# Kernel tuning notes

Hardware: AMD Instinct MI355X
Metric: run time of the kernel (lower is better)

## Reference

```python
import jax, jax.numpy as jnp
import numpy as np

G, N = 1024, 40            # graphs, nodes per graph (complete graphs)
SLOPE = 0.1                # leaky relu negative slope
SMAT_IDX = jnp.array([0, 1, 2, 3, 1, 4, 5, 6, 2, 5, 7, 8, 3, 6, 8, 9])


def setup_inputs() -> dict:
    key = jax.random.key(0)
    ks = jax.random.split(key, 24)

    # --- graph structure: G identical complete graphs of N nodes ---
    ii, jj = np.meshgrid(np.arange(N), np.arange(N), indexing="ij")
    mask = ii != jj
    src_l, dst_l = ii[mask], jj[mask]              # directed edges per graph
    offs = (np.arange(G) * N)[:, None]
    edge_index = np.stack([(src_l[None] + offs).ravel(),
                           (dst_l[None] + offs).ravel()]).astype(np.int64)
    iu, ju = np.triu_indices(N, 1)
    M = iu.shape[0]                                 # 780 undirected edges
    ud_edges = np.stack([iu, ju], 1).astype(np.int64)
    edge_map = np.zeros((N, N), np.int64)
    edge_map[iu, ju] = np.arange(M)
    edge_map[ju, iu] = np.arange(M)

    def w(k, shape, fan_in):
        return jax.random.normal(k, shape, jnp.float32) / np.sqrt(fan_in)

    inp = {
        "x": jax.random.normal(ks[0], (G * N, 16), jnp.float32),
        "edge_index": jnp.asarray(edge_index),
        "ud_edges": jnp.asarray(ud_edges),
        "edge_map": jnp.asarray(edge_map),
        # GCN stack 6->32->32->64
        "Wg0": w(ks[1], (6, 32), 6),   "bg0": jnp.zeros((32,), jnp.float32),
        "Wg1": w(ks[2], (32, 32), 32), "bg1": jnp.zeros((32,), jnp.float32),
        "Wg2": w(ks[3], (32, 64), 32), "bg2": jnp.zeros((64,), jnp.float32),
        # node MLP 64->64->64->10
        "Wn0": w(ks[4], (64, 64), 64), "bn0": jnp.zeros((64,), jnp.float32),
        "Wn1": w(ks[5], (64, 64), 64), "bn1": jnp.zeros((64,), jnp.float32),
        "Wn2": w(ks[6], (64, 10), 64), "bn2": jnp.zeros((10,), jnp.float32),
        # edge MLP 64->64->64->10
        "We0": w(ks[7], (64, 64), 64), "be0": jnp.zeros((64,), jnp.float32),
        "We1": w(ks[8], (64, 64), 64), "be1": jnp.zeros((64,), jnp.float32),
        "We2": w(ks[9], (64, 10), 64), "be2": jnp.zeros((10,), jnp.float32),
    }
    return inp


def _forward(x, edge_index, ud_edges, edge_map,
             Wg0, bg0, Wg1, bg1, Wg2, bg2,
             Wn0, bn0, Wn1, bn1, Wn2, bn2,
             We0, be0, We1, be1, We2, be2):
    num_nodes = x.shape[0]
    h = x[:, :6]                                   # node_feature_mode == 1
    src, dst = edge_index[0], edge_index[1]

    # GCN normalization (add_self_loops=False, edge_weight=1)
    deg = jax.ops.segment_sum(jnp.ones(src.shape[0], x.dtype), dst,
                              num_segments=num_nodes)
    dis = jnp.where(deg > 0, jax.lax.rsqrt(jnp.maximum(deg, 1e-12)), 0.0)
    norm = dis[src] * dis[dst]                     # [E]

    def gcn(h, W, b):
        m = (h @ W)[src] * norm[:, None]
        return jax.ops.segment_sum(m, dst, num_segments=num_nodes) + b

    # eval mode: dropout is identity
    h = jax.nn.leaky_relu(gcn(h, Wg0, bg0), SLOPE)
    h = jax.nn.leaky_relu(gcn(h, Wg1, bg1), SLOPE)
    h = gcn(h, Wg2, bg2)                           # [G*N, 64]

    hg = h.reshape(G, N, -1)                       # [G, N, 64]

    def mlp(z, Ws, bs):
        for W, b in zip(Ws[:-1], bs[:-1]):
            z = jax.nn.leaky_relu(z @ W + b, SLOPE)
        return z @ Ws[-1] + bs[-1]

    vp = mlp(hg, [Wn0, Wn1, Wn2], [bn0, bn1, bn2])            # [G, N, 10]
    e = hg[:, ud_edges[:, 0], :] + hg[:, ud_edges[:, 1], :]   # [G, M, 64]
    ep = mlp(e, [We0, We1, We2], [be0, be1, be2])             # [G, M, 10]

    # recover_X: diag blocks smat(vp[i]), off-diag smat(ep[edge_map[i,j]])
    epm = ep[:, edge_map, :]                                  # [G, N, N, 10]
    eye = jnp.eye(N, dtype=bool)[None, :, :, None]
    vecs = jnp.where(eye, vp[:, :, None, :], epm)             # [G, N, N, 10]
    blocks = vecs[..., SMAT_IDX].reshape(G, N, N, 4, 4)
    X = blocks.transpose(0, 1, 3, 2, 4).reshape(G, 4 * N, 4 * N)
    return h, X


def reference(x, edge_index, ud_edges, edge_map,
              Wg0, bg0, Wg1, bg1, Wg2, bg2,
              Wn0, bn0, Wn1, bn1, Wn2, bn2,
              We0, be0, We1, be1, We2, be2):
    return _forward(x, edge_index, ud_edges, edge_map,
                    Wg0, bg0, Wg1, bg1, Wg2, bg2,
                    Wn0, bn0, Wn1, bn1, Wn2, bn2,
                    We0, be0, We1, be1, We2, be2)
```

## Files before the change

kernel.cpp:

```cpp
#include <hip/hip_runtime.h>

#define G_GRAPHS 1024
#define N_NODES  40
#define M_EDGES  780
#define NUM_NODES (G_GRAPHS * N_NODES)
#define H_ELEMS  (NUM_NODES * 64)
#define X_STRIDE 160
#define X_PER_G  25600
#define SLOPE 0.1f

#define PACK_PER_MLP 9216

typedef __bf16 bf16x8 __attribute__((ext_vector_type(8)));
typedef unsigned short us8 __attribute__((ext_vector_type(8)));
typedef float f32x4 __attribute__((ext_vector_type(4)));

__device__ __forceinline__ float lrelu(float v) { return fmaxf(v, SLOPE * v); }
__device__ __forceinline__ unsigned short f2bf(float x) {
    __bf16 b = (__bf16)x;
    return __builtin_bit_cast(unsigned short, b);
}
__device__ __forceinline__ unsigned int pk2bf(float a, float b) {
    return (unsigned int)f2bf(a) | ((unsigned int)f2bf(b) << 16);
}

__global__ __launch_bounds__(256) void k_prep(const float* __restrict__ We0,
                                              const float* __restrict__ We1,
                                              const float* __restrict__ We2,
                                              const float* __restrict__ Wn0,
                                              const float* __restrict__ Wn1,
                                              const float* __restrict__ Wn2,
                                              unsigned short* __restrict__ wp) {
    int t = blockIdx.x * 256 + threadIdx.x;
    int mlp = t / PACK_PER_MLP;
    int o = t - mlp * PACK_PER_MLP;
    const float* W0 = mlp ? Wn0 : We0;
    const float* W1 = mlp ? Wn1 : We1;
    const float* W2 = mlp ? Wn2 : We2;
    float val;
    if (o < 8192) {
        const float* W = (o < 4096) ? W0 : W1;
        int idx = o & 4095;
        int j = idx & 7, l = (idx >> 3) & 63, tt = idx >> 9;
        int kt = tt & 1, mt = tt >> 1;
        int k = kt * 32 + ((l >> 4) & 3) * 8 + j;
        int m = mt * 16 + (l & 15);
        val = W[k * 64 + m];
    } else {
        int idx = o - 8192;
        int j = idx & 7, l = (idx >> 3) & 63, kt = idx >> 9;
        int k = kt * 32 + ((l >> 4) & 3) * 8 + j;
        int m = l & 15;
        val = (m < 10) ? W2[k * 10 + m] : 0.f;
    }
    wp[mlp * PACK_PER_MLP + o] = f2bf(val);
}

struct ChunkRegs {
    bf16x8 A1[4][2];
    bf16x8 A2[4][2];
    bf16x8 A3[2];
    float4 bv0[4];
    float4 bv1[4];
    float  bz[4];
};

__device__ __forceinline__ void run_chunk(int R0, int w, int l,
                                          const float4* sh4,
                                          unsigned short* sB,
                                          float* sEP,
                                          const ChunkRegs& cr) {
    const int nl = l & 15;
    const int rq = (l >> 4) & 3;

    {
        int rl = l >> 1, hf2 = l & 1;
        int row = R0 + rl;
        int ii = 0, jj = 0;
        bool addf = false;
        if (row < 780) {
            float tq = 6241.0f - 8.0f * (float)row;
            int i0 = (int)(0.5f * (79.0f - sqrtf(tq)));
            i0 = min(38, max(0, i0));
            int cum = 39 * i0 - ((i0 * (i0 - 1)) >> 1);
            if (cum > row) { --i0; cum = 39 * i0 - ((i0 * (i0 - 1)) >> 1); }
            else if (row - cum >= 39 - i0) { cum += 39 - i0; ++i0; }
            ii = i0; jj = i0 + 1 + (row - cum);
            addf = true;
        } else if (row >= 800 && row < 840) {
            ii = jj = row - 800;
        }
        unsigned short tmp[32];
#pragma unroll
        for (int q = 0; q < 8; q++) {
            int u = hf2 * 8 + q;
            float4 a = sh4[ii * 16 + (u ^ ((ii & 7) << 1))];
            if (addf) {
                float4 bq = sh4[jj * 16 + (u ^ ((jj & 7) << 1))];
                a.x += bq.x; a.y += bq.y; a.z += bq.z; a.w += bq.w;
            }
            tmp[4 * q + 0] = f2bf(a.x); tmp[4 * q + 1] = f2bf(a.y);
            tmp[4 * q + 2] = f2bf(a.z); tmp[4 * q + 3] = f2bf(a.w);
        }
        int r_sb = 32 * w + rl;
#pragma unroll
        for (int q = 0; q < 4; q++) {
            int cs = (hf2 * 4 + q) ^ (r_sb & 7);
            *(us8*)((char*)sB + r_sb * 128 + cs * 16) = *(const us8*)(tmp + 8 * q);
        }
    }

    auto ZB = [&](int nt, int kt) -> bf16x8 {
        int node = 32 * w + nt * 16 + nl;
        int cs = (kt * 4 + rq) ^ (node & 7);
        return __builtin_bit_cast(bf16x8,
            *(const us8*)((const char*)sB + node * 128 + cs * 16));
    };
    auto zstore = [&](int mt, int nt, const f32x4& v) {
        int node = 32 * w + nt * 16 + nl;
        int cs = (mt * 2 + (rq >> 1)) ^ (node & 7);
        uint2 u = make_uint2(pk2bf(v[0], v[1]), pk2bf(v[2], v[3]));
        *(uint2*)((char*)sB + node * 128 + cs * 16 + (rq & 1) * 8) = u;
    };

    {
        bf16x8 B[2][2];
#pragma unroll
        for (int nt = 0; nt < 2; nt++)
#pragma unroll
            for (int kt = 0; kt < 2; kt++) B[nt][kt] = ZB(nt, kt);
#pragma unroll
        for (int mt = 0; mt < 4; mt++) {
            float4 bv = cr.bv0[mt];
#pragma unroll
            for (int nt = 0; nt < 2; nt++) {
                f32x4 acc = (f32x4){0.f, 0.f, 0.f, 0.f};
                acc = __builtin_amdgcn_mfma_f32_16x16x32_bf16(cr.A1[mt][0], B[nt][0], acc, 0, 0, 0);
                acc = __builtin_amdgcn_mfma_f32_16x16x32_bf16(cr.A1[mt][1], B[nt][1], acc, 0, 0, 0);
                f32x4 z;
                z[0] = lrelu(acc[0] + bv.x); z[1] = lrelu(acc[1] + bv.y);
                z[2] = lrelu(acc[2] + bv.z); z[3] = lrelu(acc[3] + bv.w);
                zstore(mt, nt, z);
            }
        }
    }

    {
        bf16x8 B[2][2];
#pragma unroll
        for (int nt = 0; nt < 2; nt++)
#pragma unroll
            for (int kt = 0; kt < 2; kt++) B[nt][kt] = ZB(nt, kt);
#pragma unroll
        for (int mt = 0; mt < 4; mt++) {
            float4 bv = cr.bv1[mt];
#pragma unroll
            for (int nt = 0; nt < 2; nt++) {
                f32x4 acc = (f32x4){0.f, 0.f, 0.f, 0.f};
                acc = __builtin_amdgcn_mfma_f32_16x16x32_bf16(cr.A2[mt][0], B[nt][0], acc, 0, 0, 0);
                acc = __builtin_amdgcn_mfma_f32_16x16x32_bf16(cr.A2[mt][1], B[nt][1], acc, 0, 0, 0);
                f32x4 z;
                z[0] = lrelu(acc[0] + bv.x); z[1] = lrelu(acc[1] + bv.y);
                z[2] = lrelu(acc[2] + bv.z); z[3] = lrelu(acc[3] + bv.w);
                zstore(mt, nt, z);
            }
        }
    }

    {
        bf16x8 B[2][2];
#pragma unroll
        for (int nt = 0; nt < 2; nt++)
#pragma unroll
            for (int kt = 0; kt < 2; kt++) B[nt][kt] = ZB(nt, kt);
#pragma unroll
        for (int nt = 0; nt < 2; nt++) {
            f32x4 acc = (f32x4){0.f, 0.f, 0.f, 0.f};
            acc = __builtin_amdgcn_mfma_f32_16x16x32_bf16(cr.A3[0], B[nt][0], acc, 0, 0, 0);
            acc = __builtin_amdgcn_mfma_f32_16x16x32_bf16(cr.A3[1], B[nt][1], acc, 0, 0, 0);
            int rowe = R0 + nt * 16 + nl;
            bool valid = (rowe < 780) || (rowe >= 800 && rowe < 840);
            if (valid && rq < 3) {
                int epr = (rowe < 780) ? rowe : rowe - 20;
                float* p = sEP + epr * 10 + rq * 4;
                *(float2*)p = make_float2(acc[0] + cr.bz[0], acc[1] + cr.bz[1]);
                if (rq < 2)
                    *(float2*)(p + 2) = make_float2(acc[2] + cr.bz[2], acc[3] + cr.bz[3]);
            }
        }
    }
}

__global__ __launch_bounds__(256, 2) void k_fused(const float* __restrict__ x,
                                                  const float* __restrict__ Wg0,
                                                  const float* __restrict__ bg0,
                                                  const float* __restrict__ Wg1,
                                                  const float* __restrict__ bg1,
                                                  const float* __restrict__ Wg2,
                                                  const float* __restrict__ bg2,
                                                  const unsigned short* __restrict__ wp,
                                                  const float* __restrict__ be0,
                                                  const float* __restrict__ be1,
                                                  const float* __restrict__ be2,
                                                  const float* __restrict__ bn0,
                                                  const float* __restrict__ bn1,
                                                  const float* __restrict__ bn2,
                                                  float* __restrict__ hout,
                                                  float* __restrict__ X) {
    __shared__ __align__(16) char smem[59424];
    float* sh            = (float*)smem;
    unsigned short* sB   = (unsigned short*)(smem + 10240);
    float* sEP           = (float*)(smem + 26624);
    float* buf = (float*)(smem + 10240);
    float* h1  = (float*)(smem + 20480);
    float* h2  = (float*)(smem + 25600);
    float* h0  = (float*)(smem + 30720);
    float* P   = (float*)(smem + 31744);
    float* S   = (float*)(smem + 33792);

    const int g = blockIdx.x;
    const int tid = threadIdx.x;
    const int l = tid & 63;
    const int w = tid >> 6;
    const float inv39 = 1.0f / 39.0f;
    const int c32 = tid & 31;
    const int c64 = tid & 63;
    const int rq = (l >> 4) & 3;

    {
        float w0c[6], w1c[32], w2c[32];
#pragma unroll
        for (int f = 0; f < 6; f++)  w0c[f] = Wg0[f * 32 + c32];
#pragma unroll
        for (int m = 0; m < 32; m++) w1c[m] = Wg1[m * 32 + c32];
#pragma unroll
        for (int m = 0; m < 32; m++) w2c[m] = Wg2[m * 64 + c64];
        const float b0c = bg0[c32];
        const float b1c = bg1[c32];
        const float b2c = bg2[c64];

        for (int idx = tid; idx < N_NODES * 6; idx += 256) {
            int n = idx / 6, f = idx - n * 6;
            h0[idx] = x[(g * N_NODES + n) * 16 + f];
        }
        __syncthreads();

        {
            int n0 = tid >> 5;
#pragma unroll
            for (int t = 0; t < 5; t++) {
                int n = n0 + 8 * t;
                float s = 0.f;
#pragma unroll
                for (int f = 0; f < 6; f++) s += h0[n * 6 + f] * w0c[f];
                buf[n * 32 + c32] = s;
            }
        }
        __syncthreads();
        { int grp = tid >> 5; float s = 0.f;
#pragma unroll
          for (int n = grp * 5; n < grp * 5 + 5; n++) s += buf[n * 32 + c32];
          P[grp * 32 + c32] = s; }
        __syncthreads();
        if (tid < 32) { float s = 0.f;
#pragma unroll
          for (int grp = 0; grp < 8; grp++) s += P[grp * 32 + tid];
          S[tid] = s; }
        __syncthreads();
        for (int idx = tid; idx < N_NODES * 32; idx += 256)
            h1[idx] = lrelu((S[c32] - buf[idx]) * inv39 + b0c);
        __syncthreads();

        {
            int n0 = tid >> 5;
#pragma unroll
            for (int t = 0; t < 5; t++) {
                int n = n0 + 8 * t;
                const float4* hp = (const float4*)(h1 + n * 32);
                float s = 0.f;
#pragma unroll
                for (int q = 0; q < 8; q++) {
                    float4 hv = hp[q];
                    s += hv.x * w1c[4 * q + 0] + hv.y * w1c[4 * q + 1]
                       + hv.z * w1c[4 * q + 2] + hv.w * w1c[4 * q + 3];
                }
                buf[n * 32 + c32] = s;
            }
        }
        __syncthreads();
        { int grp = tid >> 5; float s = 0.f;
#pragma unroll
          for (int n = grp * 5; n < grp * 5 + 5; n++) s += buf[n * 32 + c32];
          P[grp * 32 + c32] = s; }
        __syncthreads();
        if (tid < 32) { float s = 0.f;
#pragma unroll
          for (int grp = 0; grp < 8; grp++) s += P[grp * 32 + tid];
          S[tid] = s; }
        __syncthreads();
        for (int idx = tid; idx < N_NODES * 32; idx += 256)
            h2[idx] = lrelu((S[c32] - buf[idx]) * inv39 + b1c);
        __syncthreads();

        {
            int n0 = tid >> 6;
#pragma unroll
            for (int t = 0; t < 10; t++) {
                int n = n0 + 4 * t;
                const float4* hp = (const float4*)(h2 + n * 32);
                float s = 0.f;
#pragma unroll
                for (int q = 0; q < 8; q++) {
                    float4 hv = hp[q];
                    s += hv.x * w2c[4 * q + 0] + hv.y * w2c[4 * q + 1]
                       + hv.z * w2c[4 * q + 2] + hv.w * w2c[4 * q + 3];
                }
                buf[n * 64 + c64] = s;
            }
        }
        __syncthreads();
        { int grp = tid >> 6; float s = 0.f;
#pragma unroll
          for (int n = grp * 10; n < grp * 10 + 10; n++) s += buf[n * 64 + c64];
          P[grp * 64 + c64] = s; }
        __syncthreads();
        if (tid < 64) { float s = 0.f;
#pragma unroll
          for (int grp = 0; grp < 4; grp++) s += P[grp * 64 + tid];
          S[tid] = s; }
        __syncthreads();

        for (int idx = tid; idx < N_NODES * 64; idx += 256) {
            float v = (S[c64] - buf[idx]) * inv39 + b2c;
            hout[g * N_NODES * 64 + idx] = v;
            int n = idx >> 6;
            int u = c64 >> 2;
            int us = u ^ ((n & 7) << 1);
            sh[n * 64 + us * 4 + (c64 & 3)] = v;
        }
    }
    __syncthreads();

    const float4* sh4 = (const float4*)sh;

    auto WA = [&](const unsigned short* base, int mt, int kt) -> bf16x8 {
        return __builtin_bit_cast(bf16x8,
            *(const us8*)(base + ((mt * 2 + kt) * 64 + l) * 8));
    };

    ChunkRegs ce;
#pragma unroll
    for (int mt = 0; mt < 4; mt++) {
#pragma unroll
        for (int kt = 0; kt < 2; kt++) {
            ce.A1[mt][kt] = WA(wp, mt, kt);
            ce.A2[mt][kt] = WA(wp + 4096, mt, kt);
        }
        ce.bv0[mt] = *(const float4*)(be0 + mt * 16 + rq * 4);
        ce.bv1[mt] = *(const float4*)(be1 + mt * 16 + rq * 4);
    }
    ce.A3[0] = WA(wp + 8192, 0, 0);
    ce.A3[1] = WA(wp + 8192, 0, 1);
#pragma unroll
    for (int k = 0; k < 4; k++) {
        int f = rq * 4 + k;
        ce.bz[k] = (f < 10) ? be2[f] : 0.f;
    }

    for (int c = w; c < 27; c += 4) {
        if (c < 25) {
            run_chunk(c * 32, w, l, sh4, sB, sEP, ce);
        } else {
            const unsigned short* wn = wp + PACK_PER_MLP;
            ChunkRegs cn;
#pragma unroll
            for (int mt = 0; mt < 4; mt++) {
#pragma unroll
                for (int kt = 0; kt < 2; kt++) {
                    cn.A1[mt][kt] = WA(wn, mt, kt);
                    cn.A2[mt][kt] = WA(wn + 4096, mt, kt);
                }
                cn.bv0[mt] = *(const float4*)(bn0 + mt * 16 + rq * 4);
                cn.bv1[mt] = *(const float4*)(bn1 + mt * 16 + rq * 4);
            }
            cn.A3[0] = WA(wn + 8192, 0, 0);
            cn.A3[1] = WA(wn + 8192, 0, 1);
#pragma unroll
            for (int k = 0; k < 4; k++) {
                int f = rq * 4 + k;
                cn.bz[k] = (f < 10) ? bn2[f] : 0.f;
            }
            run_chunk(c * 32, w, l, sh4, sB, sEP, cn);
        }
    }

    __syncthreads();

    float* Xg = X + g * X_PER_G;
#pragma unroll
    for (int k = 0; k < 7; k++) {
        int b = k * 256 + tid;
        if (b < 1600) {
            int bi = b / 40;
            int bj = b - bi * 40;
            int ridx;
            if (bi == bj) {
                ridx = 780 + bi;
            } else {
                int mn = min(bi, bj), mx = max(bi, bj);
                ridx = 39 * mn - ((mn * (mn - 1)) >> 1) + (mx - mn - 1);
            }
            const float* ep = sEP + ridx * 10;
            float2 e0 = *(const float2*)(ep + 0);
            float2 e1 = *(const float2*)(ep + 2);
            float2 e2 = *(const float2*)(ep + 4);
            float2 e3 = *(const float2*)(ep + 6);
            float2 e4 = *(const float2*)(ep + 8);
            float f0 = e0.x, f1 = e0.y, f2 = e1.x, f3 = e1.y;
            float f4 = e2.x, f5 = e2.y, f6 = e3.x, f7 = e3.y;
            float f8 = e4.x, f9 = e4.y;
            float4 r0 = make_float4(f0, f1, f2, f3);
            float4 r1 = make_float4(f1, f4, f5, f6);
            float4 r2 = make_float4(f2, f5, f7, f8);
            float4 r3 = make_float4(f3, f6, f8, f9);
            float* p = Xg + (4 * bi) * X_STRIDE + 4 * bj;
            *(float4*)(p + 0 * X_STRIDE) = r0;
            *(float4*)(p + 1 * X_STRIDE) = r1;
            *(float4*)(p + 2 * X_STRIDE) = r2;
            *(float4*)(p + 3 * X_STRIDE) = r3;
        }
    }
}

extern "C" void kernel_launch(void* const* d_in, const int* in_sizes, int n_in,
                              void* d_out, int out_size, void* d_ws, size_t ws_size,
                              hipStream_t stream) {
    const float* x   = (const float*)d_in[0];
    const float* Wg0 = (const float*)d_in[4];
    const float* bg0 = (const float*)d_in[5];
    const float* Wg1 = (const float*)d_in[6];
    const float* bg1 = (const float*)d_in[7];
    const float* Wg2 = (const float*)d_in[8];
    const float* bg2 = (const float*)d_in[9];
    const float* Wn0 = (const float*)d_in[10];
    const float* bn0 = (const float*)d_in[11];
    const float* Wn1 = (const float*)d_in[12];
    const float* bn1 = (const float*)d_in[13];
    const float* Wn2 = (const float*)d_in[14];
    const float* bn2 = (const float*)d_in[15];
    const float* We0 = (const float*)d_in[16];
    const float* be0 = (const float*)d_in[17];
    const float* We1 = (const float*)d_in[18];
    const float* be1 = (const float*)d_in[19];
    const float* We2 = (const float*)d_in[20];
    const float* be2 = (const float*)d_in[21];

    float* hout = (float*)d_out;
    float* X    = hout + H_ELEMS;
    unsigned short* wp = (unsigned short*)d_ws;

    k_prep<<<72, 256, 0, stream>>>(We0, We1, We2, Wn0, Wn1, Wn2, wp);
    k_fused<<<G_GRAPHS, 256, 0, stream>>>(x, Wg0, bg0, Wg1, bg1, Wg2, bg2,
                                          wp, be0, be1, be2, bn0, bn1, bn2,
                                          hout, X);
}
```

Baseline: 234.0 us.

## Scatter X blocks per chunk from a per-wave buffer to cut LDS and raise occupancy

Each wave now writes its chunk's edge and node MLP outputs into a small per-wave LDS scratch and immediately scatters the symmetric 4x4 blocks to X. This removes the whole-graph sEP staging buffer, the final block barrier and the separate recover pass. LDS drops from about 58KB to 32KB, and launch bounds rise from 2 to 4 blocks per CU to use the freed space. The risks are register pressure under the tighter launch bound, since the weight registers are now reloaded in place. The X writes are also more scattered, with each edge's two mirrored blocks written by lane pairs.

```diff
diff --git a/kernel.cpp b/kernel.cpp
--- a/kernel.cpp
+++ b/kernel.cpp
@@ -68,34 +68,37 @@
 __device__ __forceinline__ void run_chunk(int R0, int w, int l,
                                           const float4* sh4,
                                           unsigned short* sB,
-                                          float* sEP,
+                                          float* miniw,
+                                          float* Xg,
                                           const ChunkRegs& cr) {
     const int nl = l & 15;
     const int rq = (l >> 4) & 3;
-
-    {
-        int rl = l >> 1, hf2 = l & 1;
-        int row = R0 + rl;
-        int ii = 0, jj = 0;
-        bool addf = false;
-        if (row < 780) {
-            float tq = 6241.0f - 8.0f * (float)row;
-            int i0 = (int)(0.5f * (79.0f - sqrtf(tq)));
-            i0 = min(38, max(0, i0));
-            int cum = 39 * i0 - ((i0 * (i0 - 1)) >> 1);
-            if (cum > row) { --i0; cum = 39 * i0 - ((i0 * (i0 - 1)) >> 1); }
-            else if (row - cum >= 39 - i0) { cum += 39 - i0; ++i0; }
-            ii = i0; jj = i0 + 1 + (row - cum);
-            addf = true;
-        } else if (row >= 800 && row < 840) {
-            ii = jj = row - 800;
-        }
+    const int rl = l >> 1;
+    const int hf2 = l & 1;
+    const int row = R0 + rl;
+
+    const bool is_e = (row < 780);
+    const bool is_n = (row >= 800 && row < 840);
+    int ii = 0, jj = 0;
+    if (is_e) {
+        float tq = 6241.0f - 8.0f * (float)row;
+        int i0 = (int)(0.5f * (79.0f - sqrtf(tq)));
+        i0 = min(38, max(0, i0));
+        int cum = 39 * i0 - ((i0 * (i0 - 1)) >> 1);
+        if (cum > row) { --i0; cum = 39 * i0 - ((i0 * (i0 - 1)) >> 1); }
+        else if (row - cum >= 39 - i0) { cum += 39 - i0; ++i0; }
+        ii = i0; jj = i0 + 1 + (row - cum);
+    } else if (is_n) {
+        ii = jj = row - 800;
+    }
+
+    {
         unsigned short tmp[32];
 #pragma unroll
         for (int q = 0; q < 8; q++) {
             int u = hf2 * 8 + q;
             float4 a = sh4[ii * 16 + (u ^ ((ii & 7) << 1))];
-            if (addf) {
+            if (is_e) {
                 float4 bq = sh4[jj * 16 + (u ^ ((jj & 7) << 1))];
                 a.x += bq.x; a.y += bq.y; a.z += bq.z; a.w += bq.w;
             }
@@ -178,20 +181,51 @@
             f32x4 acc = (f32x4){0.f, 0.f, 0.f, 0.f};
             acc = __builtin_amdgcn_mfma_f32_16x16x32_bf16(cr.A3[0], B[nt][0], acc, 0, 0, 0);
             acc = __builtin_amdgcn_mfma_f32_16x16x32_bf16(cr.A3[1], B[nt][1], acc, 0, 0, 0);
-            int rowe = R0 + nt * 16 + nl;
-            bool valid = (rowe < 780) || (rowe >= 800 && rowe < 840);
-            if (valid && rq < 3) {
-                int epr = (rowe < 780) ? rowe : rowe - 20;
-                float* p = sEP + epr * 10 + rq * 4;
+            int rl2 = nt * 16 + nl;
+            if (rq < 3) {
+                float* p = miniw + rl2 * 12 + rq * 4;
                 *(float2*)p = make_float2(acc[0] + cr.bz[0], acc[1] + cr.bz[1]);
                 if (rq < 2)
                     *(float2*)(p + 2) = make_float2(acc[2] + cr.bz[2], acc[3] + cr.bz[3]);
             }
         }
     }
-}
-
-__global__ __launch_bounds__(256, 2) void k_fused(const float* __restrict__ x,
+
+    {
+        const float* ep = miniw + rl * 12;
+        float2 e0 = *(const float2*)(ep + 0);
+        float2 e1 = *(const float2*)(ep + 2);
+        float2 e2 = *(const float2*)(ep + 4);
+        float2 e3 = *(const float2*)(ep + 6);
+        float2 e4 = *(const float2*)(ep + 8);
+        float f0 = e0.x, f1 = e0.y, f2 = e1.x, f3 = e1.y;
+        float f4 = e2.x, f5 = e2.y, f6 = e3.x, f7 = e3.y;
+        float f8 = e4.x, f9 = e4.y;
+        float4 r0 = make_float4(f0, f1, f2, f3);
+        float4 r1 = make_float4(f1, f4, f5, f6);
+        float4 r2 = make_float4(f2, f5, f7, f8);
+        float4 r3 = make_float4(f3, f6, f8, f9);
+        if (is_e) {
+            int bi = hf2 ? jj : ii, bj = hf2 ? ii : jj;
+            float* p = Xg + (4 * bi) * X_STRIDE + 4 * bj;
+            *(float4*)(p + 0 * X_STRIDE) = r0;
+            *(float4*)(p + 1 * X_STRIDE) = r1;
+            *(float4*)(p + 2 * X_STRIDE) = r2;
+            *(float4*)(p + 3 * X_STRIDE) = r3;
+        } else if (is_n) {
+            float* p = Xg + (4 * ii + hf2 * 2) * X_STRIDE + 4 * ii;
+            if (hf2 == 0) {
+                *(float4*)(p + 0 * X_STRIDE) = r0;
+                *(float4*)(p + 1 * X_STRIDE) = r1;
+            } else {
+                *(float4*)(p + 0 * X_STRIDE) = r2;
+                *(float4*)(p + 1 * X_STRIDE) = r3;
+            }
+        }
+    }
+}
+
+__global__ __launch_bounds__(256, 4) void k_fused(const float* __restrict__ x,
                                                   const float* __restrict__ Wg0,
                                                   const float* __restrict__ bg0,
                                                   const float* __restrict__ Wg1,
@@ -207,16 +241,16 @@
                                                   const float* __restrict__ bn2,
                                                   float* __restrict__ hout,
                                                   float* __restrict__ X) {
-    __shared__ __align__(16) char smem[59424];
-    float* sh            = (float*)smem;
-    unsigned short* sB   = (unsigned short*)(smem + 10240);
-    float* sEP           = (float*)(smem + 26624);
+    __shared__ __align__(16) char smem[32768];
+    float* sh          = (float*)smem;
+    unsigned short* sB = (unsigned short*)(smem + 10240);
+    float* mini        = (float*)(smem + 26624);
+    float* h0  = (float*)smem;
+    float* P   = (float*)(smem + 1024);
     float* buf = (float*)(smem + 10240);
     float* h1  = (float*)(smem + 20480);
-    float* h2  = (float*)(smem + 25600);
-    float* h0  = (float*)(smem + 30720);
-    float* P   = (float*)(smem + 31744);
-    float* S   = (float*)(smem + 33792);
+    float* S   = (float*)(smem + 25600);
+    float* h2  = (float*)(smem + 26624);
 
     const int g = blockIdx.x;
     const int tid = threadIdx.x;
@@ -342,93 +376,41 @@
     __syncthreads();
 
     const float4* sh4 = (const float4*)sh;
+    float* miniw = mini + w * 384;
+    float* Xg = X + g * X_PER_G;
 
     auto WA = [&](const unsigned short* base, int mt, int kt) -> bf16x8 {
         return __builtin_bit_cast(bf16x8,
             *(const us8*)(base + ((mt * 2 + kt) * 64 + l) * 8));
     };
+    auto loadW = [&](ChunkRegs& cr, const unsigned short* wb,
+                     const float* B0, const float* B1, const float* B2) {
+#pragma unroll
+        for (int mt = 0; mt < 4; mt++) {
+#pragma unroll
+            for (int kt = 0; kt < 2; kt++) {
+                cr.A1[mt][kt] = WA(wb, mt, kt);
+                cr.A2[mt][kt] = WA(wb + 4096, mt, kt);
+            }
+            cr.bv0[mt] = *(const float4*)(B0 + mt * 16 + rq * 4);
+            cr.bv1[mt] = *(const float4*)(B1 + mt * 16 + rq * 4);
+        }
+        cr.A3[0] = WA(wb + 8192, 0, 0);
+        cr.A3[1] = WA(wb + 8192, 0, 1);
+#pragma unroll
+        for (int k = 0; k < 4; k++) {
+            int f = rq * 4 + k;
+            cr.bz[k] = (f < 10) ? B2[f] : 0.f;
+        }
+    };
 
     ChunkRegs ce;
-#pragma unroll
-    for (int mt = 0; mt < 4; mt++) {
-#pragma unroll
-        for (int kt = 0; kt < 2; kt++) {
-            ce.A1[mt][kt] = WA(wp, mt, kt);
-            ce.A2[mt][kt] = WA(wp + 4096, mt, kt);
-        }
-        ce.bv0[mt] = *(const float4*)(be0 + mt * 16 + rq * 4);
-        ce.bv1[mt] = *(const float4*)(be1 + mt * 16 + rq * 4);
-    }
-    ce.A3[0] = WA(wp + 8192, 0, 0);
-    ce.A3[1] = WA(wp + 8192, 0, 1);
-#pragma unroll
-    for (int k = 0; k < 4; k++) {
-        int f = rq * 4 + k;
-        ce.bz[k] = (f < 10) ? be2[f] : 0.f;
-    }
+    loadW(ce, wp, be0, be1, be2);
 
     for (int c = w; c < 27; c += 4) {
-        if (c < 25) {
-            run_chunk(c * 32, w, l, sh4, sB, sEP, ce);
-        } else {
-            const unsigned short* wn = wp + PACK_PER_MLP;
-            ChunkRegs cn;
-#pragma unroll
-            for (int mt = 0; mt < 4; mt++) {
-#pragma unroll
-                for (int kt = 0; kt < 2; kt++) {
-                    cn.A1[mt][kt] = WA(wn, mt, kt);
-                    cn.A2[mt][kt] = WA(wn + 4096, mt, kt);
-                }
-                cn.bv0[mt] = *(const float4*)(bn0 + mt * 16 + rq * 4);
-                cn.bv1[mt] = *(const float4*)(bn1 + mt * 16 + rq * 4);
-            }
-            cn.A3[0] = WA(wn + 8192, 0, 0);
-            cn.A3[1] = WA(wn + 8192, 0, 1);
-#pragma unroll
-            for (int k = 0; k < 4; k++) {
-                int f = rq * 4 + k;
-                cn.bz[k] = (f < 10) ? bn2[f] : 0.f;
-            }
-            run_chunk(c * 32, w, l, sh4, sB, sEP, cn);
-        }
-    }
-
-    __syncthreads();
-
-    float* Xg = X + g * X_PER_G;
-#pragma unroll
-    for (int k = 0; k < 7; k++) {
-        int b = k * 256 + tid;
-        if (b < 1600) {
-            int bi = b / 40;
-            int bj = b - bi * 40;
-            int ridx;
-            if (bi == bj) {
-                ridx = 780 + bi;
-            } else {
-                int mn = min(bi, bj), mx = max(bi, bj);
-                ridx = 39 * mn - ((mn * (mn - 1)) >> 1) + (mx - mn - 1);
-            }
-            const float* ep = sEP + ridx * 10;
-            float2 e0 = *(const float2*)(ep + 0);
-            float2 e1 = *(const float2*)(ep + 2);
-            float2 e2 = *(const float2*)(ep + 4);
-            float2 e3 = *(const float2*)(ep + 6);
-            float2 e4 = *(const float2*)(ep + 8);
-            float f0 = e0.x, f1 = e0.y, f2 = e1.x, f3 = e1.y;
-            float f4 = e2.x, f5 = e2.y, f6 = e3.x, f7 = e3.y;
-            float f8 = e4.x, f9 = e4.y;
-            float4 r0 = make_float4(f0, f1, f2, f3);
-            float4 r1 = make_float4(f1, f4, f5, f6);
-            float4 r2 = make_float4(f2, f5, f7, f8);
-            float4 r3 = make_float4(f3, f6, f8, f9);
-            float* p = Xg + (4 * bi) * X_STRIDE + 4 * bj;
-            *(float4*)(p + 0 * X_STRIDE) = r0;
-            *(float4*)(p + 1 * X_STRIDE) = r1;
-            *(float4*)(p + 2 * X_STRIDE) = r2;
-            *(float4*)(p + 3 * X_STRIDE) = r3;
-        }
+        if (c >= 25)
+            loadW(ce, wp + PACK_PER_MLP, bn0, bn1, bn2);
+        run_chunk(c * 32, w, l, sh4, sB, miniw, Xg, ce);
     }
 }
 
```

After: 292.5 us. +25.0%, slower.
